# Performance work log

Measured on AMD Instinct MI355X. Metric: run time of the kernel, lower is better.

The kernel has to match this reference:

```python
import jax, jax.numpy as jnp
import numpy as np

N_NODES = 50000
IN_DIM = 128
HIDDEN = 64
OUT_DIM = 3
HEADS1 = 4
NEG_SLOPE = 0.2
EPS = 1e-16


def _glorot(key, shape):
    fan_in, fan_out = shape[0], shape[-1]
    lim = (6.0 / (fan_in + fan_out)) ** 0.5
    return jax.random.uniform(key, shape, jnp.float32, -lim, lim)


def setup_inputs() -> dict:
    key = jax.random.key(0)
    ks = jax.random.split(key, 12)
    x = jax.random.normal(ks[0], (N_NODES, IN_DIM), jnp.float32)
    edge_index = jax.random.randint(ks[1], (2, 400000), 0, N_NODES, jnp.int64)
    # layer 1: GATConv(in=128, out=64, heads=4)
    W1 = _glorot(ks[2], (IN_DIM, HEADS1 * HIDDEN))
    att_src1 = _glorot(ks[3], (HEADS1, HIDDEN))
    att_dst1 = _glorot(ks[4], (HEADS1, HIDDEN))
    b1 = jnp.zeros((HEADS1 * HIDDEN,), jnp.float32)
    # layer 2: GATConv(in=256, out=64, heads=1)
    W2 = _glorot(ks[5], (HEADS1 * HIDDEN, HIDDEN))
    att_src2 = _glorot(ks[6], (1, HIDDEN))
    att_dst2 = _glorot(ks[7], (1, HIDDEN))
    b2 = jnp.zeros((HIDDEN,), jnp.float32)
    # output linear
    Wout = _glorot(ks[8], (HIDDEN, OUT_DIM))
    bout = jnp.zeros((OUT_DIM,), jnp.float32)
    return {"x": x, "edge_index": edge_index, "W1": W1, "att_src1": att_src1,
            "att_dst1": att_dst1, "b1": b1, "W2": W2, "att_src2": att_src2,
            "att_dst2": att_dst2, "b2": b2, "Wout": Wout, "bout": bout}


def gat_conv(x, src, dst, W, a_src, a_dst, b, n_nodes):
    H, C = a_src.shape
    h = (x @ W).reshape(n_nodes, H, C)            # [N,H,C]
    a_s = jnp.sum(h * a_src[None], axis=-1)        # [N,H]
    a_d = jnp.sum(h * a_dst[None], axis=-1)        # [N,H]
    e = jax.nn.leaky_relu(a_s[src] + a_d[dst], NEG_SLOPE)  # [E,H]
    # segment softmax over incoming edges of each dst node
    m = jax.ops.segment_max(e, dst, num_segments=n_nodes)
    ex = jnp.exp(e - m[dst])
    denom = jax.ops.segment_sum(ex, dst, num_segments=n_nodes)
    alpha = ex / (denom[dst] + EPS)                # [E,H]
    msg = h[src] * alpha[..., None]                # [E,H,C]
    out = jax.ops.segment_sum(msg, dst, num_segments=n_nodes)
    return out.reshape(n_nodes, H * C) + b


def reference(x, edge_index, W1, att_src1, att_dst1, b1, W2, att_src2, att_dst2, b2, Wout, bout):
    n = x.shape[0]
    loop = jnp.arange(n, dtype=edge_index.dtype)
    src = jnp.concatenate([edge_index[0], loop])   # add self loops (PyG default)
    dst = jnp.concatenate([edge_index[1], loop])
    h = gat_conv(x, src, dst, W1, att_src1, att_dst1, b1, n)
    h = jax.nn.elu(h)
    h = gat_conv(h, src, dst, W2, att_src2, att_dst2, b2, n)
    h = jax.nn.elu(h)
    return h @ Wout + bout
```

## Files before the change

kernel.cpp:

```cpp
#include <hip/hip_runtime.h>
#include <hip/hip_bf16.h>
#include <math.h>

#define N_NODES  50000
#define IN_DIM   128
#define HIDDEN   64
#define OUT_DIM  3
#define HEADS1   4
#define E_RAW    400000
#define E_TOT    450000
#define NEG_SLOPE 0.2f
#define SCAN_CHUNK 1024
#define N_CHUNKS ((N_NODES + SCAN_CHUNK - 1) / SCAN_CHUNK)
#define WPREP_BLOCKS 128

typedef __attribute__((ext_vector_type(8))) short bf16x8;
typedef __attribute__((ext_vector_type(4))) float f32x4;

static __device__ __forceinline__ float bfu(unsigned short u) {
    return __uint_as_float(((unsigned)u) << 16);
}
static __device__ __forceinline__ unsigned short f2b_bits(float v) {
    __hip_bfloat16 b = __float2bfloat16(v);
    return *reinterpret_cast<unsigned short*>(&b);
}

static __device__ __forceinline__ void get_edge(const int* __restrict__ ei, int is64,
                                                int e, int& s, int& d) {
    if (e >= E_RAW) { s = d = e - E_RAW; return; }
    if (is64) { s = ei[2 * e]; d = ei[2 * E_RAW + 2 * e]; }
    else      { s = ei[e];     d = ei[E_RAW + e]; }
    s = min(max(s, 0), N_NODES - 1);
    d = min(max(d, 0), N_NODES - 1);
}

__global__ void detect_int64_kernel(const int* __restrict__ ei, int* __restrict__ flag) {
    __shared__ int any_nonzero;
    if (threadIdx.x == 0) any_nonzero = 0;
    __syncthreads();
    for (int i = threadIdx.x; i < 8192; i += blockDim.x) {
        int k = i * 48;
        if (ei[2 * k + 1] != 0) any_nonzero = 1;
    }
    __syncthreads();
    if (threadIdx.x == 0) flag[0] = (any_nonzero == 0) ? 1 : 0;
}

__global__ void wprep_count_kernel(const float* __restrict__ W1, __hip_bfloat16* __restrict__ W1T,
                                   const float* __restrict__ W2, __hip_bfloat16* __restrict__ W2T,
                                   const int* __restrict__ ei, const int* __restrict__ flag,
                                   int* __restrict__ deg) {
    int bid = blockIdx.x;
    if (bid < WPREP_BLOCKS) {
        int i = bid * 256 + threadIdx.x;
        if (i < 256 * 128) {
            int n = i >> 7, k = i & 127;
            *((unsigned short*)W1T + i) = f2b_bits(W1[k * 256 + n]);
        }
        if (i < 64 * 256) {
            int n = i >> 8, k = i & 255;
            *((unsigned short*)W2T + i) = f2b_bits(W2[k * 64 + n]);
        }
        return;
    }
    int e = (bid - WPREP_BLOCKS) * 256 + threadIdx.x;
    if (e >= E_TOT) return;
    int s, d;
    get_edge(ei, flag[0], e, s, d);
    atomicAdd(&deg[d], 1);
}

__global__ void scan_local_kernel(const int* __restrict__ deg, int* __restrict__ row_ptr,
                                  int* __restrict__ bsums) {
    __shared__ int buf[SCAN_CHUNK];
    int base = blockIdx.x * SCAN_CHUNK;
    int i = base + threadIdx.x;
    buf[threadIdx.x] = (i < N_NODES) ? deg[i] : 0;
    __syncthreads();
    for (int off = 1; off < SCAN_CHUNK; off <<= 1) {
        int t = (threadIdx.x >= off) ? buf[threadIdx.x - off] : 0;
        __syncthreads();
        buf[threadIdx.x] += t;
        __syncthreads();
    }
    if (i < N_NODES) row_ptr[i + 1] = buf[threadIdx.x];
    if (threadIdx.x == SCAN_CHUNK - 1) bsums[blockIdx.x] = buf[SCAN_CHUNK - 1];
    if (blockIdx.x == 0 && threadIdx.x == 0) row_ptr[0] = 0;
}

__global__ void scan_bsums_kernel(int* __restrict__ bsums) {
    __shared__ int buf[64];
    int i = threadIdx.x;
    buf[i] = (i < N_CHUNKS) ? bsums[i] : 0;
    __syncthreads();
    for (int off = 1; off < 64; off <<= 1) {
        int t = (i >= off) ? buf[i - off] : 0;
        __syncthreads();
        buf[i] += t;
        __syncthreads();
    }
    if (i < N_CHUNKS) bsums[i] = (i == 0) ? 0 : buf[i - 1];
}

__global__ void scan_add_kernel(int* __restrict__ row_ptr, const int* __restrict__ bsums,
                                const int* __restrict__ deg, int* __restrict__ cursor) {
    int i = blockIdx.x * blockDim.x + threadIdx.x;
    if (i < N_NODES) {
        int incl = row_ptr[i + 1] + bsums[i / SCAN_CHUNK];
        row_ptr[i + 1] = incl;
        cursor[i] = incl - deg[i];
    }
}

__global__ void scatter_kernel(const int* __restrict__ ei, const int* __restrict__ flag,
                               int* __restrict__ cursor, int* __restrict__ csr_src) {
    int e = blockIdx.x * blockDim.x + threadIdx.x;
    if (e >= E_TOT) return;
    int s, d;
    get_edge(ei, flag[0], e, s, d);
    int pos = atomicAdd(&cursor[d], 1);
    csr_src[pos] = s;
}

__global__ void __launch_bounds__(256) gemm_l1_mfma_kernel(
        const float* __restrict__ x, const __hip_bfloat16* __restrict__ W1T,
        const float* __restrict__ att_s, const float* __restrict__ att_d,
        __hip_bfloat16* __restrict__ h1,
        float* __restrict__ asb4, float* __restrict__ adb4) {
    __shared__ unsigned short As[16][136];
    const int tid = threadIdx.x;
    const int wave = tid >> 6, lane = tid & 63;
    const int quad = lane >> 4, m = lane & 15;
    const int row0 = blockIdx.x * 16;
    {
        int r = tid >> 4, seg = tid & 15;
        const float* xa = x + (size_t)(row0 + r) * IN_DIM + seg * 8;
        float4 u = *(const float4*)xa;
        float4 v = *(const float4*)(xa + 4);
        ushort4 p0, p1;
        p0.x = f2b_bits(u.x); p0.y = f2b_bits(u.y); p0.z = f2b_bits(u.z); p0.w = f2b_bits(u.w);
        p1.x = f2b_bits(v.x); p1.y = f2b_bits(v.y); p1.z = f2b_bits(v.z); p1.w = f2b_bits(v.w);
        *(ushort4*)&As[r][seg * 8]     = p0;
        *(ushort4*)&As[r][seg * 8 + 4] = p1;
    }
    __syncthreads();
    const int n0w = wave * 64;
    f32x4 acc0 = {0.f, 0.f, 0.f, 0.f}, acc1 = acc0, acc2 = acc0, acc3 = acc0;
    #pragma unroll
    for (int k0 = 0; k0 < IN_DIM; k0 += 32) {
        int kk = k0 + quad * 8;
        bf16x8 a = *(const bf16x8*)&As[m][kk];
        bf16x8 b0 = *(const bf16x8*)(W1T + (size_t)(n0w +  0 + m) * IN_DIM + kk);
        bf16x8 b1 = *(const bf16x8*)(W1T + (size_t)(n0w + 16 + m) * IN_DIM + kk);
        bf16x8 b2 = *(const bf16x8*)(W1T + (size_t)(n0w + 32 + m) * IN_DIM + kk);
        bf16x8 b3 = *(const bf16x8*)(W1T + (size_t)(n0w + 48 + m) * IN_DIM + kk);
        acc0 = __builtin_amdgcn_mfma_f32_16x16x32_bf16(a, b0, acc0, 0, 0, 0);
        acc1 = __builtin_amdgcn_mfma_f32_16x16x32_bf16(a, b1, acc1, 0, 0, 0);
        acc2 = __builtin_amdgcn_mfma_f32_16x16x32_bf16(a, b2, acc2, 0, 0, 0);
        acc3 = __builtin_amdgcn_mfma_f32_16x16x32_bf16(a, b3, acc3, 0, 0, 0);
    }
    float ats0 = att_s[n0w +  0 + m], atd0 = att_d[n0w +  0 + m];
    float ats1 = att_s[n0w + 16 + m], atd1 = att_d[n0w + 16 + m];
    float ats2 = att_s[n0w + 32 + m], atd2 = att_d[n0w + 32 + m];
    float ats3 = att_s[n0w + 48 + m], atd3 = att_d[n0w + 48 + m];
    unsigned short* out = (unsigned short*)h1;
    #pragma unroll
    for (int i = 0; i < 4; i++) {
        int grow = row0 + quad * 4 + i;
        size_t base = (size_t)grow * 256;
        out[base + n0w +  0 + m] = f2b_bits(acc0[i]);
        out[base + n0w + 16 + m] = f2b_bits(acc1[i]);
        out[base + n0w + 32 + m] = f2b_bits(acc2[i]);
        out[base + n0w + 48 + m] = f2b_bits(acc3[i]);
        float ps = acc0[i] * ats0 + acc1[i] * ats1 + acc2[i] * ats2 + acc3[i] * ats3;
        float pd = acc0[i] * atd0 + acc1[i] * atd1 + acc2[i] * atd2 + acc3[i] * atd3;
        #pragma unroll
        for (int off = 1; off < 16; off <<= 1) {
            ps += __shfl_xor(ps, off, 16);
            pd += __shfl_xor(pd, off, 16);
        }
        if (m == 0) {
            asb4[grow * 4 + wave] = ps;
            adb4[grow * 4 + wave] = pd;
        }
    }
}

__global__ void __launch_bounds__(256) gemm_l2_mfma_kernel(
        const __hip_bfloat16* __restrict__ eluagg, const __hip_bfloat16* __restrict__ W2T,
        const float* __restrict__ att_s, const float* __restrict__ att_d,
        __hip_bfloat16* __restrict__ h2,
        float* __restrict__ asb, float* __restrict__ adb) {
    __shared__ float sPS[4][16];
    __shared__ float sPD[4][16];
    const int tid = threadIdx.x;
    const int wave = tid >> 6, lane = tid & 63;
    const int quad = lane >> 4, m = lane & 15;
    const int row0 = blockIdx.x * 16;
    const int n0 = wave * 16;
    f32x4 acc = {0.f, 0.f, 0.f, 0.f};
    #pragma unroll
    for (int k0 = 0; k0 < 256; k0 += 32) {
        int kk = k0 + quad * 8;
        bf16x8 a = *(const bf16x8*)(eluagg + (size_t)(row0 + m) * 256 + kk);
        bf16x8 b = *(const bf16x8*)(W2T + (size_t)(n0 + m) * 256 + kk);
        acc = __builtin_amdgcn_mfma_f32_16x16x32_bf16(a, b, acc, 0, 0, 0);
    }
    float ats = att_s[n0 + m], atd = att_d[n0 + m];
    unsigned short* out = (unsigned short*)h2;
    #pragma unroll
    for (int i = 0; i < 4; i++) {
        int grow = row0 + quad * 4 + i;
        out[(size_t)grow * 64 + n0 + m] = f2b_bits(acc[i]);
        float ps = acc[i] * ats;
        float pd = acc[i] * atd;
        #pragma unroll
        for (int off = 1; off < 16; off <<= 1) {
            ps += __shfl_xor(ps, off, 16);
            pd += __shfl_xor(pd, off, 16);
        }
        if (m == 0) {
            sPS[wave][quad * 4 + i] = ps;
            sPD[wave][quad * 4 + i] = pd;
        }
    }
    __syncthreads();
    if (tid < 16) {
        float ps = sPS[0][tid] + sPS[1][tid] + sPS[2][tid] + sPS[3][tid];
        float pd = sPD[0][tid] + sPD[1][tid] + sPD[2][tid] + sPD[3][tid];
        asb[row0 + tid] = ps;
        adb[row0 + tid] = pd;
    }
}

__global__ void __launch_bounds__(256) gat_gather4_kernel(
        const int* __restrict__ row_ptr, const int* __restrict__ csr_src,
        const float* __restrict__ asb4, const float* __restrict__ adb4,
        const __hip_bfloat16* __restrict__ h1, const float* __restrict__ bias,
        __hip_bfloat16* __restrict__ eluagg) {
    int wave = threadIdx.x >> 6;
    int lane = threadIdx.x & 63;
    int n = blockIdx.x * 4 + wave;
    if (n >= N_NODES) return;
    int b = row_ptr[n], e = row_ptr[n + 1];
    const int c    = lane & 31;
    const int slot = lane >> 5;
    const int head = c >> 3;
    const int ei   = lane >> 2;
    const int hh   = lane & 3;
    float adnh = adb4[n * 4 + hh];
    float acc[8];
    #pragma unroll
    for (int i = 0; i < 8; i++) acc[i] = 0.f;
    float l = 0.f;
    for (int c0 = b; c0 < e; c0 += 16) {
        int cnt = min(16, e - c0);
        int s_all = (lane < cnt) ? csr_src[c0 + lane] : 0;
        int sE = __shfl(s_all, ei, 64);
        float w_all = 0.f;
        if (ei < cnt) {
            float v = asb4[sE * 4 + hh] + adnh;
            v = (v > 0.f) ? v : NEG_SLOPE * v;
            w_all = __expf(v);
        }
        #pragma unroll 2
        for (int k = 0; k < cnt; k += 2) {
            int eidx = k + slot;
            int s = __shfl(s_all, eidx, 64);
            float w = __shfl(w_all, eidx * 4 + head, 64);
            bf16x8 f = *(const bf16x8*)(h1 + (size_t)s * 256 + c * 8);
            l += w;
            #pragma unroll
            for (int i = 0; i < 8; i++)
                acc[i] += w * bfu((unsigned short)f[i]);
        }
    }
    #pragma unroll
    for (int i = 0; i < 8; i++) acc[i] += __shfl_xor(acc[i], 32, 64);
    l += __shfl_xor(l, 32, 64);
    if (lane < 32) {
        float il = 1.f / (l + 1e-16f);
        float4 b0 = *(const float4*)(bias + c * 8);
        float4 b1 = *(const float4*)(bias + c * 8 + 4);
        float r[8];
        r[0] = acc[0] * il + b0.x; r[1] = acc[1] * il + b0.y;
        r[2] = acc[2] * il + b0.z; r[3] = acc[3] * il + b0.w;
        r[4] = acc[4] * il + b1.x; r[5] = acc[5] * il + b1.y;
        r[6] = acc[6] * il + b1.z; r[7] = acc[7] * il + b1.w;
        bf16x8 st;
        #pragma unroll
        for (int i = 0; i < 8; i++) {
            float v = (r[i] > 0.f) ? r[i] : expm1f(r[i]);
            st[i] = (short)f2b_bits(v);
        }
        *(bf16x8*)(eluagg + (size_t)n * 256 + c * 8) = st;
    }
}

__global__ void __launch_bounds__(256) gat_gather1_out_kernel(
        const int* __restrict__ row_ptr, const int* __restrict__ csr_src,
        const float* __restrict__ asb, const float* __restrict__ adb,
        const __hip_bfloat16* __restrict__ h2, const float* __restrict__ bias,
        const float* __restrict__ Wout, const float* __restrict__ bout,
        float* __restrict__ out) {
    int wave = threadIdx.x >> 6;
    int lane = threadIdx.x & 63;
    int n = blockIdx.x * 4 + wave;
    if (n >= N_NODES) return;
    int b = row_ptr[n], e = row_ptr[n + 1];
    const int c    = lane & 7;
    const int slot = lane >> 3;
    float adn = adb[n];
    float acc[8];
    #pragma unroll
    for (int i = 0; i < 8; i++) acc[i] = 0.f;
    float l = 0.f;
    for (int c0 = b; c0 < e; c0 += 64) {
        int cnt = min(64, e - c0);
        int s_all = (lane < cnt) ? csr_src[c0 + lane] : 0;
        float w_all = 0.f;
        if (lane < cnt) {
            float v = asb[s_all] + adn;
            v = (v > 0.f) ? v : NEG_SLOPE * v;
            w_all = __expf(v);
        }
        #pragma unroll 2
        for (int k = 0; k < cnt; k += 8) {
            int eidx = k + slot;
            int s = __shfl(s_all, eidx, 64);
            float w = __shfl(w_all, eidx, 64);
            bf16x8 f = *(const bf16x8*)(h2 + (size_t)s * 64 + c * 8);
            l += w;
            #pragma unroll
            for (int i = 0; i < 8; i++)
                acc[i] += w * bfu((unsigned short)f[i]);
        }
    }
    #pragma unroll
    for (int off = 8; off < 64; off <<= 1) {
        #pragma unroll
        for (int i = 0; i < 8; i++) acc[i] += __shfl_xor(acc[i], off, 64);
        l += __shfl_xor(l, off, 64);
    }
    float il = 1.f / (l + 1e-16f);
    float4 b0 = *(const float4*)(bias + c * 8);
    float4 b1 = *(const float4*)(bias + c * 8 + 4);
    float v[8];
    v[0] = acc[0] * il + b0.x; v[1] = acc[1] * il + b0.y;
    v[2] = acc[2] * il + b0.z; v[3] = acc[3] * il + b0.w;
    v[4] = acc[4] * il + b1.x; v[5] = acc[5] * il + b1.y;
    v[6] = acc[6] * il + b1.z; v[7] = acc[7] * il + b1.w;
    #pragma unroll
    for (int i = 0; i < 8; i++) v[i] = (v[i] > 0.f) ? v[i] : expm1f(v[i]);
    const float* wp = Wout + c * 24;
    float o0 = 0.f, o1 = 0.f, o2 = 0.f;
    #pragma unroll
    for (int i = 0; i < 8; i++) {
        o0 += v[i] * wp[i * 3 + 0];
        o1 += v[i] * wp[i * 3 + 1];
        o2 += v[i] * wp[i * 3 + 2];
    }
    #pragma unroll
    for (int off = 1; off < 8; off <<= 1) {
        o0 += __shfl_xor(o0, off, 64);
        o1 += __shfl_xor(o1, off, 64);
        o2 += __shfl_xor(o2, off, 64);
    }
    if (lane == 0) {
        out[n * OUT_DIM + 0] = o0 + bout[0];
        out[n * OUT_DIM + 1] = o1 + bout[1];
        out[n * OUT_DIM + 2] = o2 + bout[2];
    }
}

extern "C" void kernel_launch(void* const* d_in, const int* in_sizes, int n_in,
                              void* d_out, int out_size, void* d_ws, size_t ws_size,
                              hipStream_t stream) {
    const float* x    = (const float*)d_in[0];
    const int*   ei   = (const int*)d_in[1];
    const float* W1   = (const float*)d_in[2];
    const float* as1  = (const float*)d_in[3];
    const float* ad1  = (const float*)d_in[4];
    const float* b1   = (const float*)d_in[5];
    const float* W2   = (const float*)d_in[6];
    const float* as2  = (const float*)d_in[7];
    const float* ad2  = (const float*)d_in[8];
    const float* b2v  = (const float*)d_in[9];
    const float* Wout = (const float*)d_in[10];
    const float* bout = (const float*)d_in[11];
    float* out = (float*)d_out;

    float* ws    = (float*)d_ws;
    int*   flag  = (int*)ws;
    float* asb4  = ws + 16;
    float* adb4  = asb4 + (size_t)N_NODES * 4;
    float* asb1  = adb4 + (size_t)N_NODES * 4;
    float* adb1  = asb1 + N_NODES;
    __hip_bfloat16* h1     = (__hip_bfloat16*)(adb1 + N_NODES);
    __hip_bfloat16* eluagg = (__hip_bfloat16*)(h1 + (size_t)N_NODES * 256);
    __hip_bfloat16* h2     = (__hip_bfloat16*)(eluagg + (size_t)N_NODES * 256);
    __hip_bfloat16* W1T    = (__hip_bfloat16*)(h2 + (size_t)N_NODES * 64);
    __hip_bfloat16* W2T    = W1T + 256 * 128;
    int* deg     = (int*)(W2T + 64 * 256);
    int* bsums   = deg + N_NODES;
    int* row_ptr = bsums + 64;
    int* cursor  = row_ptr + N_NODES + 16;
    int* csr_src = cursor + N_NODES;

    const int EB = (E_TOT + 255) / 256;
    const int NB = (N_NODES + 255) / 256;
    const int AB = (N_NODES + 3) / 4;
    const int MB = N_NODES / 16;

    detect_int64_kernel<<<1, 256, 0, stream>>>(ei, flag);
    hipMemsetAsync(deg, 0, (size_t)N_NODES * sizeof(int), stream);

    wprep_count_kernel<<<WPREP_BLOCKS + EB, 256, 0, stream>>>(W1, W1T, W2, W2T, ei, flag, deg);
    scan_local_kernel<<<N_CHUNKS, SCAN_CHUNK, 0, stream>>>(deg, row_ptr, bsums);
    scan_bsums_kernel<<<1, 64, 0, stream>>>(bsums);
    scan_add_kernel<<<NB, 256, 0, stream>>>(row_ptr, bsums, deg, cursor);
    scatter_kernel<<<EB, 256, 0, stream>>>(ei, flag, cursor, csr_src);

    gemm_l1_mfma_kernel<<<MB, 256, 0, stream>>>(x, W1T, as1, ad1, h1, asb4, adb4);
    gat_gather4_kernel<<<AB, 256, 0, stream>>>(row_ptr, csr_src, asb4, adb4, h1, b1, eluagg);

    gemm_l2_mfma_kernel<<<MB, 256, 0, stream>>>(eluagg, W2T, as2, ad2, h2, asb1, adb1);
    gat_gather1_out_kernel<<<AB, 256, 0, stream>>>(row_ptr, csr_src, asb1, adb1, h2,
                                                   b2v, Wout, bout, out);
}
```

Measured before the change: 284.9 us.

## Store layer-1 features head-major and split gather blocks per head

The layer-1 GEMM now writes h1 and the attention logits in a head-major layout ([head][node][64] and [head][node]). The gather kernel gets one block per (head, 8-node group), so each wave reads 128-byte rows from a single head's plane. The intent is to shrink the working set that must stay in cache per pass, at the cost of 4x more blocks and an extra cross-lane reduction. The int64-detection kernel is also parallelised across 32 blocks, with a memset initialising the flag.

Measured after the change: 326.5 us. 1.15x slower.

```diff
diff --git a/kernel.cpp b/kernel.cpp
--- a/kernel.cpp
+++ b/kernel.cpp
@@ -13,6 +13,7 @@
 #define SCAN_CHUNK 1024
 #define N_CHUNKS ((N_NODES + SCAN_CHUNK - 1) / SCAN_CHUNK)
 #define WPREP_BLOCKS 128
+#define G4_BLOCKS 50000
 
 typedef __attribute__((ext_vector_type(8))) short bf16x8;
 typedef __attribute__((ext_vector_type(4))) float f32x4;
@@ -35,15 +36,9 @@
 }
 
 __global__ void detect_int64_kernel(const int* __restrict__ ei, int* __restrict__ flag) {
-    __shared__ int any_nonzero;
-    if (threadIdx.x == 0) any_nonzero = 0;
-    __syncthreads();
-    for (int i = threadIdx.x; i < 8192; i += blockDim.x) {
-        int k = i * 48;
-        if (ei[2 * k + 1] != 0) any_nonzero = 1;
-    }
-    __syncthreads();
-    if (threadIdx.x == 0) flag[0] = (any_nonzero == 0) ? 1 : 0;
+    int i = blockIdx.x * blockDim.x + threadIdx.x;
+    int k = i * 48;
+    if (ei[2 * k + 1] != 0) flag[0] = 0;
 }
 
 __global__ void wprep_count_kernel(const float* __restrict__ W1, __hip_bfloat16* __restrict__ W1T,
@@ -164,14 +159,15 @@
     float ats2 = att_s[n0w + 32 + m], atd2 = att_d[n0w + 32 + m];
     float ats3 = att_s[n0w + 48 + m], atd3 = att_d[n0w + 48 + m];
     unsigned short* out = (unsigned short*)h1;
+    const size_t hbase = (size_t)wave * N_NODES * 64;
     #pragma unroll
     for (int i = 0; i < 4; i++) {
         int grow = row0 + quad * 4 + i;
-        size_t base = (size_t)grow * 256;
-        out[base + n0w +  0 + m] = f2b_bits(acc0[i]);
-        out[base + n0w + 16 + m] = f2b_bits(acc1[i]);
-        out[base + n0w + 32 + m] = f2b_bits(acc2[i]);
-        out[base + n0w + 48 + m] = f2b_bits(acc3[i]);
+        size_t base = hbase + (size_t)grow * 64;
+        out[base +  0 + m] = f2b_bits(acc0[i]);
+        out[base + 16 + m] = f2b_bits(acc1[i]);
+        out[base + 32 + m] = f2b_bits(acc2[i]);
+        out[base + 48 + m] = f2b_bits(acc3[i]);
         float ps = acc0[i] * ats0 + acc1[i] * ats1 + acc2[i] * ats2 + acc3[i] * ats3;
         float pd = acc0[i] * atd0 + acc1[i] * atd1 + acc2[i] * atd2 + acc3[i] * atd3;
         #pragma unroll
@@ -180,8 +176,8 @@
             pd += __shfl_xor(pd, off, 16);
         }
         if (m == 0) {
-            asb4[grow * 4 + wave] = ps;
-            adb4[grow * 4 + wave] = pd;
+            asb4[(size_t)wave * N_NODES + grow] = ps;
+            adb4[(size_t)wave * N_NODES + grow] = pd;
         }
     }
 }
@@ -236,39 +232,42 @@
 __global__ void __launch_bounds__(256) gat_gather4_kernel(
         const int* __restrict__ row_ptr, const int* __restrict__ csr_src,
         const float* __restrict__ asb4, const float* __restrict__ adb4,
-        const __hip_bfloat16* __restrict__ h1, const float* __restrict__ bias,
+        const __hip_bfloat16* __restrict__ h1,
+        const float* __restrict__ bias,
         __hip_bfloat16* __restrict__ eluagg) {
-    int wave = threadIdx.x >> 6;
-    int lane = threadIdx.x & 63;
-    int n = blockIdx.x * 4 + wave;
+    const int bid  = blockIdx.x;
+    const int x    = bid & 7;
+    const int head = x >> 1;
+    const int nb   = (bid >> 3) * 2 + (x & 1);
+    const int wave = threadIdx.x >> 6;
+    const int lane = threadIdx.x & 63;
+    const int n = nb * 4 + wave;
     if (n >= N_NODES) return;
     int b = row_ptr[n], e = row_ptr[n + 1];
-    const int c    = lane & 31;
-    const int slot = lane >> 5;
-    const int head = c >> 3;
-    const int ei   = lane >> 2;
-    const int hh   = lane & 3;
-    float adnh = adb4[n * 4 + hh];
+    const int c    = lane & 7;
+    const int slot = lane >> 3;
+    const __hip_bfloat16* h1h = h1 + (size_t)head * N_NODES * 64;
+    const float* asbh = asb4 + (size_t)head * N_NODES;
+    const float adn = adb4[(size_t)head * N_NODES + n];
     float acc[8];
     #pragma unroll
     for (int i = 0; i < 8; i++) acc[i] = 0.f;
     float l = 0.f;
-    for (int c0 = b; c0 < e; c0 += 16) {
-        int cnt = min(16, e - c0);
+    for (int c0 = b; c0 < e; c0 += 64) {
+        int cnt = min(64, e - c0);
         int s_all = (lane < cnt) ? csr_src[c0 + lane] : 0;
-        int sE = __shfl(s_all, ei, 64);
         float w_all = 0.f;
-        if (ei < cnt) {
-            float v = asb4[sE * 4 + hh] + adnh;
+        if (lane < cnt) {
+            float v = asbh[s_all] + adn;
             v = (v > 0.f) ? v : NEG_SLOPE * v;
             w_all = __expf(v);
         }
         #pragma unroll 2
-        for (int k = 0; k < cnt; k += 2) {
+        for (int k = 0; k < cnt; k += 8) {
             int eidx = k + slot;
             int s = __shfl(s_all, eidx, 64);
-            float w = __shfl(w_all, eidx * 4 + head, 64);
-            bf16x8 f = *(const bf16x8*)(h1 + (size_t)s * 256 + c * 8);
+            float w = __shfl(w_all, eidx, 64);
+            bf16x8 f = *(const bf16x8*)(h1h + (size_t)s * 64 + c * 8);
             l += w;
             #pragma unroll
             for (int i = 0; i < 8; i++)
@@ -276,12 +275,15 @@
         }
     }
     #pragma unroll
-    for (int i = 0; i < 8; i++) acc[i] += __shfl_xor(acc[i], 32, 64);
-    l += __shfl_xor(l, 32, 64);
-    if (lane < 32) {
+    for (int off = 8; off < 64; off <<= 1) {
+        #pragma unroll
+        for (int i = 0; i < 8; i++) acc[i] += __shfl_xor(acc[i], off, 64);
+        l += __shfl_xor(l, off, 64);
+    }
+    if (lane < 8) {
         float il = 1.f / (l + 1e-16f);
-        float4 b0 = *(const float4*)(bias + c * 8);
-        float4 b1 = *(const float4*)(bias + c * 8 + 4);
+        float4 b0 = *(const float4*)(bias + head * 64 + c * 8);
+        float4 b1 = *(const float4*)(bias + head * 64 + c * 8 + 4);
         float r[8];
         r[0] = acc[0] * il + b0.x; r[1] = acc[1] * il + b0.y;
         r[2] = acc[2] * il + b0.z; r[3] = acc[3] * il + b0.w;
@@ -293,7 +295,7 @@
             float v = (r[i] > 0.f) ? r[i] : expm1f(r[i]);
             st[i] = (short)f2b_bits(v);
         }
-        *(bf16x8*)(eluagg + (size_t)n * 256 + c * 8) = st;
+        *(bf16x8*)(eluagg + (size_t)n * 256 + head * 64 + c * 8) = st;
     }
 }
 
@@ -412,7 +414,8 @@
     const int AB = (N_NODES + 3) / 4;
     const int MB = N_NODES / 16;
 
-    detect_int64_kernel<<<1, 256, 0, stream>>>(ei, flag);
+    hipMemsetAsync(flag, 1, 4, stream);
+    detect_int64_kernel<<<32, 256, 0, stream>>>(ei, flag);
     hipMemsetAsync(deg, 0, (size_t)N_NODES * sizeof(int), stream);
 
     wprep_count_kernel<<<WPREP_BLOCKS + EB, 256, 0, stream>>>(W1, W1T, W2, W2T, ei, flag, deg);
@@ -422,7 +425,7 @@
     scatter_kernel<<<EB, 256, 0, stream>>>(ei, flag, cursor, csr_src);
 
     gemm_l1_mfma_kernel<<<MB, 256, 0, stream>>>(x, W1T, as1, ad1, h1, asb4, adb4);
-    gat_gather4_kernel<<<AB, 256, 0, stream>>>(row_ptr, csr_src, asb4, adb4, h1, b1, eluagg);
+    gat_gather4_kernel<<<G4_BLOCKS, 256, 0, stream>>>(row_ptr, csr_src, asb4, adb4, h1, b1, eluagg);
 
     gemm_l2_mfma_kernel<<<MB, 256, 0, stream>>>(eluagg, W2T, as2, ad2, h2, asb1, adb1);
     gat_gather1_out_kernel<<<AB, 256, 0, stream>>>(row_ptr, csr_src, asb1, adb1, h2,
```

## Fuse layer-1 gather with layer-2 GEMM and fold small scan/memset kernels

Applied to the files above, without the earlier changes.

Layer-1 attention aggregation now runs inside the layer-2 GEMM kernel. Each block aggregates 16 nodes into shared memory and feeds them straight to MFMA, so the 25.6MB eluagg intermediate is never written to or read back from global memory. The degree memset is folded into the int64-detect kernel, and the bsums scan is moved into scan_add via wave shuffles, removing two launches. The cost is that each block now handles 16 nodes sequentially, four per wave, which lowers parallelism during the latency-bound gather phase and adds a block barrier before the MFMA.

Measured after the change: 267.7 us. -6.1%, faster.

```diff
diff --git a/kernel.cpp b/kernel.cpp
--- a/kernel.cpp
+++ b/kernel.cpp
@@ -34,16 +34,24 @@
     d = min(max(d, 0), N_NODES - 1);
 }
 
-__global__ void detect_int64_kernel(const int* __restrict__ ei, int* __restrict__ flag) {
-    __shared__ int any_nonzero;
-    if (threadIdx.x == 0) any_nonzero = 0;
-    __syncthreads();
-    for (int i = threadIdx.x; i < 8192; i += blockDim.x) {
-        int k = i * 48;
-        if (ei[2 * k + 1] != 0) any_nonzero = 1;
-    }
-    __syncthreads();
-    if (threadIdx.x == 0) flag[0] = (any_nonzero == 0) ? 1 : 0;
+__global__ void detect_zero_kernel(const int* __restrict__ ei, int* __restrict__ flag,
+                                   int* __restrict__ deg) {
+    int gid = blockIdx.x * 256 + threadIdx.x;
+    for (int i = gid; i < N_NODES; i += 64 * 256) deg[i] = 0;
+    if (blockIdx.x == 0) {
+        int nz = 0;
+        #pragma unroll 4
+        for (int t = 0; t < 32; t++) {
+            int k = (threadIdx.x * 32 + t) * 48;
+            nz |= ei[2 * k + 1];
+        }
+        __shared__ int s;
+        if (threadIdx.x == 0) s = 0;
+        __syncthreads();
+        if (__any(nz != 0) && (threadIdx.x & 63) == 0) s = 1;
+        __syncthreads();
+        if (threadIdx.x == 0) flag[0] = s ? 0 : 1;
+    }
 }
 
 __global__ void wprep_count_kernel(const float* __restrict__ W1, __hip_bfloat16* __restrict__ W1T,
@@ -88,25 +96,24 @@
     if (blockIdx.x == 0 && threadIdx.x == 0) row_ptr[0] = 0;
 }
 
-__global__ void scan_bsums_kernel(int* __restrict__ bsums) {
-    __shared__ int buf[64];
-    int i = threadIdx.x;
-    buf[i] = (i < N_CHUNKS) ? bsums[i] : 0;
-    __syncthreads();
-    for (int off = 1; off < 64; off <<= 1) {
-        int t = (i >= off) ? buf[i - off] : 0;
-        __syncthreads();
-        buf[i] += t;
-        __syncthreads();
-    }
-    if (i < N_CHUNKS) bsums[i] = (i == 0) ? 0 : buf[i - 1];
-}
-
 __global__ void scan_add_kernel(int* __restrict__ row_ptr, const int* __restrict__ bsums,
                                 const int* __restrict__ deg, int* __restrict__ cursor) {
+    __shared__ int soff[64];
+    if (threadIdx.x < 64) {
+        int v = (threadIdx.x < N_CHUNKS) ? bsums[threadIdx.x] : 0;
+        #pragma unroll
+        for (int off = 1; off < 64; off <<= 1) {
+            int t = __shfl_up(v, off, 64);
+            if (threadIdx.x >= off) v += t;
+        }
+        soff[threadIdx.x] = v;
+    }
+    __syncthreads();
     int i = blockIdx.x * blockDim.x + threadIdx.x;
     if (i < N_NODES) {
-        int incl = row_ptr[i + 1] + bsums[i / SCAN_CHUNK];
+        int ch = i / SCAN_CHUNK;
+        int add = (ch == 0) ? 0 : soff[ch - 1];
+        int incl = row_ptr[i + 1] + add;
         row_ptr[i + 1] = incl;
         cursor[i] = incl - deg[i];
     }
@@ -186,25 +193,88 @@
     }
 }
 
-__global__ void __launch_bounds__(256) gemm_l2_mfma_kernel(
-        const __hip_bfloat16* __restrict__ eluagg, const __hip_bfloat16* __restrict__ W2T,
+__global__ void __launch_bounds__(256) gat_gather4_l2_kernel(
+        const int* __restrict__ row_ptr, const int* __restrict__ csr_src,
+        const float* __restrict__ asb4, const float* __restrict__ adb4,
+        const __hip_bfloat16* __restrict__ h1, const float* __restrict__ bias,
+        const __hip_bfloat16* __restrict__ W2T,
         const float* __restrict__ att_s, const float* __restrict__ att_d,
         __hip_bfloat16* __restrict__ h2,
         float* __restrict__ asb, float* __restrict__ adb) {
+    __shared__ unsigned short As[16][264];
     __shared__ float sPS[4][16];
     __shared__ float sPD[4][16];
     const int tid = threadIdx.x;
     const int wave = tid >> 6, lane = tid & 63;
+    const int row0 = blockIdx.x * 16;
+    const int c    = lane & 31;
+    const int slot = lane >> 5;
+    const int head = c >> 3;
+    const int eidx0 = lane >> 2;
+    const int hh   = lane & 3;
+
+    for (int g = 0; g < 4; g++) {
+        const int n = row0 + wave * 4 + g;
+        int b = row_ptr[n], e = row_ptr[n + 1];
+        float adnh = adb4[n * 4 + hh];
+        float acc[8];
+        #pragma unroll
+        for (int i = 0; i < 8; i++) acc[i] = 0.f;
+        float l = 0.f;
+        for (int c0 = b; c0 < e; c0 += 16) {
+            int cnt = min(16, e - c0);
+            int s_all = (lane < cnt) ? csr_src[c0 + lane] : 0;
+            int sE = __shfl(s_all, eidx0, 64);
+            float w_all = 0.f;
+            if (eidx0 < cnt) {
+                float v = asb4[sE * 4 + hh] + adnh;
+                v = (v > 0.f) ? v : NEG_SLOPE * v;
+                w_all = __expf(v);
+            }
+            #pragma unroll 2
+            for (int k = 0; k < cnt; k += 2) {
+                int eidx = k + slot;
+                int s = __shfl(s_all, eidx, 64);
+                float w = __shfl(w_all, eidx * 4 + head, 64);
+                bf16x8 f = *(const bf16x8*)(h1 + (size_t)s * 256 + c * 8);
+                l += w;
+                #pragma unroll
+                for (int i = 0; i < 8; i++)
+                    acc[i] += w * bfu((unsigned short)f[i]);
+            }
+        }
+        #pragma unroll
+        for (int i = 0; i < 8; i++) acc[i] += __shfl_xor(acc[i], 32, 64);
+        l += __shfl_xor(l, 32, 64);
+        if (lane < 32) {
+            float il = 1.f / (l + 1e-16f);
+            float4 b0 = *(const float4*)(bias + c * 8);
+            float4 b1 = *(const float4*)(bias + c * 8 + 4);
+            float r[8];
+            r[0] = acc[0] * il + b0.x; r[1] = acc[1] * il + b0.y;
+            r[2] = acc[2] * il + b0.z; r[3] = acc[3] * il + b0.w;
+            r[4] = acc[4] * il + b1.x; r[5] = acc[5] * il + b1.y;
+            r[6] = acc[6] * il + b1.z; r[7] = acc[7] * il + b1.w;
+            bf16x8 st;
+            #pragma unroll
+            for (int i = 0; i < 8; i++) {
+                float v = (r[i] > 0.f) ? r[i] : expm1f(r[i]);
+                st[i] = (short)f2b_bits(v);
+            }
+            *(bf16x8*)&As[wave * 4 + g][c * 8] = st;
+        }
+    }
+    __syncthreads();
+
     const int quad = lane >> 4, m = lane & 15;
-    const int row0 = blockIdx.x * 16;
     const int n0 = wave * 16;
     f32x4 acc = {0.f, 0.f, 0.f, 0.f};
     #pragma unroll
     for (int k0 = 0; k0 < 256; k0 += 32) {
         int kk = k0 + quad * 8;
-        bf16x8 a = *(const bf16x8*)(eluagg + (size_t)(row0 + m) * 256 + kk);
-        bf16x8 b = *(const bf16x8*)(W2T + (size_t)(n0 + m) * 256 + kk);
-        acc = __builtin_amdgcn_mfma_f32_16x16x32_bf16(a, b, acc, 0, 0, 0);
+        bf16x8 a = *(const bf16x8*)&As[m][kk];
+        bf16x8 bfr = *(const bf16x8*)(W2T + (size_t)(n0 + m) * 256 + kk);
+        acc = __builtin_amdgcn_mfma_f32_16x16x32_bf16(a, bfr, acc, 0, 0, 0);
     }
     float ats = att_s[n0 + m], atd = att_d[n0 + m];
     unsigned short* out = (unsigned short*)h2;
@@ -230,70 +300,6 @@
         float pd = sPD[0][tid] + sPD[1][tid] + sPD[2][tid] + sPD[3][tid];
         asb[row0 + tid] = ps;
         adb[row0 + tid] = pd;
-    }
-}
-
-__global__ void __launch_bounds__(256) gat_gather4_kernel(
-        const int* __restrict__ row_ptr, const int* __restrict__ csr_src,
-        const float* __restrict__ asb4, const float* __restrict__ adb4,
-        const __hip_bfloat16* __restrict__ h1, const float* __restrict__ bias,
-        __hip_bfloat16* __restrict__ eluagg) {
-    int wave = threadIdx.x >> 6;
-    int lane = threadIdx.x & 63;
-    int n = blockIdx.x * 4 + wave;
-    if (n >= N_NODES) return;
-    int b = row_ptr[n], e = row_ptr[n + 1];
-    const int c    = lane & 31;
-    const int slot = lane >> 5;
-    const int head = c >> 3;
-    const int ei   = lane >> 2;
-    const int hh   = lane & 3;
-    float adnh = adb4[n * 4 + hh];
-    float acc[8];
-    #pragma unroll
-    for (int i = 0; i < 8; i++) acc[i] = 0.f;
-    float l = 0.f;
-    for (int c0 = b; c0 < e; c0 += 16) {
-        int cnt = min(16, e - c0);
-        int s_all = (lane < cnt) ? csr_src[c0 + lane] : 0;
-        int sE = __shfl(s_all, ei, 64);
-        float w_all = 0.f;
-        if (ei < cnt) {
-            float v = asb4[sE * 4 + hh] + adnh;
-            v = (v > 0.f) ? v : NEG_SLOPE * v;
-            w_all = __expf(v);
-        }
-        #pragma unroll 2
-        for (int k = 0; k < cnt; k += 2) {
-            int eidx = k + slot;
-            int s = __shfl(s_all, eidx, 64);
-            float w = __shfl(w_all, eidx * 4 + head, 64);
-            bf16x8 f = *(const bf16x8*)(h1 + (size_t)s * 256 + c * 8);
-            l += w;
-            #pragma unroll
-            for (int i = 0; i < 8; i++)
-                acc[i] += w * bfu((unsigned short)f[i]);
-        }
-    }
-    #pragma unroll
-    for (int i = 0; i < 8; i++) acc[i] += __shfl_xor(acc[i], 32, 64);
-    l += __shfl_xor(l, 32, 64);
-    if (lane < 32) {
-        float il = 1.f / (l + 1e-16f);
-        float4 b0 = *(const float4*)(bias + c * 8);
-        float4 b1 = *(const float4*)(bias + c * 8 + 4);
-        float r[8];
-        r[0] = acc[0] * il + b0.x; r[1] = acc[1] * il + b0.y;
-        r[2] = acc[2] * il + b0.z; r[3] = acc[3] * il + b0.w;
-        r[4] = acc[4] * il + b1.x; r[5] = acc[5] * il + b1.y;
-        r[6] = acc[6] * il + b1.z; r[7] = acc[7] * il + b1.w;
-        bf16x8 st;
-        #pragma unroll
-        for (int i = 0; i < 8; i++) {
-            float v = (r[i] > 0.f) ? r[i] : expm1f(r[i]);
-            st[i] = (short)f2b_bits(v);
-        }
-        *(bf16x8*)(eluagg + (size_t)n * 256 + c * 8) = st;
     }
 }
 
@@ -397,8 +403,7 @@
     float* asb1  = adb4 + (size_t)N_NODES * 4;
     float* adb1  = asb1 + N_NODES;
     __hip_bfloat16* h1     = (__hip_bfloat16*)(adb1 + N_NODES);
-    __hip_bfloat16* eluagg = (__hip_bfloat16*)(h1 + (size_t)N_NODES * 256);
-    __hip_bfloat16* h2     = (__hip_bfloat16*)(eluagg + (size_t)N_NODES * 256);
+    __hip_bfloat16* h2     = (__hip_bfloat16*)(h1 + (size_t)N_NODES * 256);
     __hip_bfloat16* W1T    = (__hip_bfloat16*)(h2 + (size_t)N_NODES * 64);
     __hip_bfloat16* W2T    = W1T + 256 * 128;
     int* deg     = (int*)(W2T + 64 * 256);
@@ -412,19 +417,17 @@
     const int AB = (N_NODES + 3) / 4;
     const int MB = N_NODES / 16;
 
-    detect_int64_kernel<<<1, 256, 0, stream>>>(ei, flag);
-    hipMemsetAsync(deg, 0, (size_t)N_NODES * sizeof(int), stream);
-
+    detect_zero_kernel<<<64, 256, 0, stream>>>(ei, flag, deg);
     wprep_count_kernel<<<WPREP_BLOCKS + EB, 256, 0, stream>>>(W1, W1T, W2, W2T, ei, flag, deg);
     scan_local_kernel<<<N_CHUNKS, SCAN_CHUNK, 0, stream>>>(deg, row_ptr, bsums);
-    scan_bsums_kernel<<<1, 64, 0, stream>>>(bsums);
     scan_add_kernel<<<NB, 256, 0, stream>>>(row_ptr, bsums, deg, cursor);
     scatter_kernel<<<EB, 256, 0, stream>>>(ei, flag, cursor, csr_src);
 
     gemm_l1_mfma_kernel<<<MB, 256, 0, stream>>>(x, W1T, as1, ad1, h1, asb4, adb4);
-    gat_gather4_kernel<<<AB, 256, 0, stream>>>(row_ptr, csr_src, asb4, adb4, h1, b1, eluagg);
-
-    gemm_l2_mfma_kernel<<<MB, 256, 0, stream>>>(eluagg, W2T, as2, ad2, h2, asb1, adb1);
+
+    gat_gather4_l2_kernel<<<MB, 256, 0, stream>>>(row_ptr, csr_src, asb4, adb4, h1, b1,
+                                                  W2T, as2, ad2, h2, asb1, adb1);
+
     gat_gather1_out_kernel<<<AB, 256, 0, stream>>>(row_ptr, csr_src, asb1, adb1, h2,
                                                    b2v, Wout, bout, out);
 }
```

## Merge preprocessing kernels: per-block int64 detect, single-block scan, fused scatter+GEMM1

Applied to the files above, without the earlier changes.

Drops the separate int64-detection kernel; each edge block now infers the index width from the high words of its own edges. The three-kernel multi-block prefix scan becomes one single-block kernel that walks the degree array in 49 chunks using wave shuffles and a running carry. The CSR scatter is merged into the layer-1 GEMM launch as extra blocks so the two overlap. This removes several launches and serialization points, but the single-block scan runs serially over 50k entries. Per-block width detection may also be wrong if a block's high words happen to be all zero.

Measured after the change: 297.3 us. +4.3%, slower.

```diff
diff --git a/kernel.cpp b/kernel.cpp
--- a/kernel.cpp
+++ b/kernel.cpp
@@ -10,9 +10,9 @@
 #define E_RAW    400000
 #define E_TOT    450000
 #define NEG_SLOPE 0.2f
-#define SCAN_CHUNK 1024
-#define N_CHUNKS ((N_NODES + SCAN_CHUNK - 1) / SCAN_CHUNK)
 #define WPREP_BLOCKS 128
+#define EB_SC ((E_TOT + 255) / 256)
+#define MB_GE (N_NODES / 16)
 
 typedef __attribute__((ext_vector_type(8))) short bf16x8;
 typedef __attribute__((ext_vector_type(4))) float f32x4;
@@ -34,22 +34,21 @@
     d = min(max(d, 0), N_NODES - 1);
 }
 
-__global__ void detect_int64_kernel(const int* __restrict__ ei, int* __restrict__ flag) {
-    __shared__ int any_nonzero;
-    if (threadIdx.x == 0) any_nonzero = 0;
+static __device__ __forceinline__ int block_is64(const int* __restrict__ ei,
+                                                 int e, bool valid, int* nzbuf) {
+    bool real = valid && (e < E_RAW);
+    int hv = real ? ei[2 * e + 1] : 0;
+    if (threadIdx.x == 0) *nzbuf = 0;
     __syncthreads();
-    for (int i = threadIdx.x; i < 8192; i += blockDim.x) {
-        int k = i * 48;
-        if (ei[2 * k + 1] != 0) any_nonzero = 1;
-    }
+    if (__any(hv != 0) && (threadIdx.x & 63) == 0) *nzbuf = 1;
     __syncthreads();
-    if (threadIdx.x == 0) flag[0] = (any_nonzero == 0) ? 1 : 0;
+    return (*nzbuf == 0);
 }
 
 __global__ void wprep_count_kernel(const float* __restrict__ W1, __hip_bfloat16* __restrict__ W1T,
                                    const float* __restrict__ W2, __hip_bfloat16* __restrict__ W2T,
-                                   const int* __restrict__ ei, const int* __restrict__ flag,
-                                   int* __restrict__ deg) {
+                                   const int* __restrict__ ei, int* __restrict__ deg) {
+    __shared__ int nz;
     int bid = blockIdx.x;
     if (bid < WPREP_BLOCKS) {
         int i = bid * 256 + threadIdx.x;
@@ -64,74 +63,72 @@
         return;
     }
     int e = (bid - WPREP_BLOCKS) * 256 + threadIdx.x;
-    if (e >= E_TOT) return;
+    bool valid = e < E_TOT;
+    int is64 = block_is64(ei, e, valid, &nz);
+    if (!valid) return;
     int s, d;
-    get_edge(ei, flag[0], e, s, d);
+    get_edge(ei, is64, e, s, d);
     atomicAdd(&deg[d], 1);
 }
 
-__global__ void scan_local_kernel(const int* __restrict__ deg, int* __restrict__ row_ptr,
-                                  int* __restrict__ bsums) {
-    __shared__ int buf[SCAN_CHUNK];
-    int base = blockIdx.x * SCAN_CHUNK;
-    int i = base + threadIdx.x;
-    buf[threadIdx.x] = (i < N_NODES) ? deg[i] : 0;
-    __syncthreads();
-    for (int off = 1; off < SCAN_CHUNK; off <<= 1) {
-        int t = (threadIdx.x >= off) ? buf[threadIdx.x - off] : 0;
+__global__ void scan_all_kernel(const int* __restrict__ deg, int* __restrict__ row_ptr,
+                                int* __restrict__ cursor) {
+    __shared__ int wsum[4];
+    const int t = threadIdx.x, wv = t >> 6, ln = t & 63;
+    int carry = 0;
+    if (t == 0) row_ptr[0] = 0;
+    for (int chunk = 0; chunk < 49; ++chunk) {
+        int g = chunk * 256 + t;
+        int4 d = (g < 12500) ? ((const int4*)deg)[g] : make_int4(0, 0, 0, 0);
+        int p0 = d.x, p1 = p0 + d.y, p2 = p1 + d.z, p3 = p2 + d.w;
+        int s = p3;
+        #pragma unroll
+        for (int off = 1; off < 64; off <<= 1) {
+            int u = __shfl_up(s, off, 64);
+            if (ln >= off) s += u;
+        }
+        if (ln == 63) wsum[wv] = s;
         __syncthreads();
-        buf[threadIdx.x] += t;
+        int wbase = carry;
+        #pragma unroll
+        for (int w = 0; w < 4; w++) wbase += (w < wv) ? wsum[w] : 0;
+        int ex = wbase + s - p3;
+        if (g < 12500) {
+            int i = g * 4;
+            row_ptr[i + 1] = ex + p0; row_ptr[i + 2] = ex + p1;
+            row_ptr[i + 3] = ex + p2; row_ptr[i + 4] = ex + p3;
+            cursor[i]     = ex;       cursor[i + 1]  = ex + p0;
+            cursor[i + 2] = ex + p1;  cursor[i + 3]  = ex + p2;
+        }
+        carry += wsum[0] + wsum[1] + wsum[2] + wsum[3];
         __syncthreads();
     }
-    if (i < N_NODES) row_ptr[i + 1] = buf[threadIdx.x];
-    if (threadIdx.x == SCAN_CHUNK - 1) bsums[blockIdx.x] = buf[SCAN_CHUNK - 1];
-    if (blockIdx.x == 0 && threadIdx.x == 0) row_ptr[0] = 0;
-}
-
-__global__ void scan_bsums_kernel(int* __restrict__ bsums) {
-    __shared__ int buf[64];
-    int i = threadIdx.x;
-    buf[i] = (i < N_CHUNKS) ? bsums[i] : 0;
-    __syncthreads();
-    for (int off = 1; off < 64; off <<= 1) {
-        int t = (i >= off) ? buf[i - off] : 0;
-        __syncthreads();
-        buf[i] += t;
-        __syncthreads();
-    }
-    if (i < N_CHUNKS) bsums[i] = (i == 0) ? 0 : buf[i - 1];
-}
-
-__global__ void scan_add_kernel(int* __restrict__ row_ptr, const int* __restrict__ bsums,
-                                const int* __restrict__ deg, int* __restrict__ cursor) {
-    int i = blockIdx.x * blockDim.x + threadIdx.x;
-    if (i < N_NODES) {
-        int incl = row_ptr[i + 1] + bsums[i / SCAN_CHUNK];
-        row_ptr[i + 1] = incl;
-        cursor[i] = incl - deg[i];
-    }
-}
-
-__global__ void scatter_kernel(const int* __restrict__ ei, const int* __restrict__ flag,
-                               int* __restrict__ cursor, int* __restrict__ csr_src) {
-    int e = blockIdx.x * blockDim.x + threadIdx.x;
-    if (e >= E_TOT) return;
-    int s, d;
-    get_edge(ei, flag[0], e, s, d);
-    int pos = atomicAdd(&cursor[d], 1);
-    csr_src[pos] = s;
-}
-
-__global__ void __launch_bounds__(256) gemm_l1_mfma_kernel(
+}
+
+__global__ void __launch_bounds__(256) scatter_gemm_l1_kernel(
+        const int* __restrict__ ei,
+        int* __restrict__ cursor, int* __restrict__ csr_src,
         const float* __restrict__ x, const __hip_bfloat16* __restrict__ W1T,
         const float* __restrict__ att_s, const float* __restrict__ att_d,
         __hip_bfloat16* __restrict__ h1,
         float* __restrict__ asb4, float* __restrict__ adb4) {
     __shared__ unsigned short As[16][136];
+    __shared__ int nz;
+    if (blockIdx.x < EB_SC) {
+        int e = blockIdx.x * 256 + threadIdx.x;
+        bool valid = e < E_TOT;
+        int is64 = block_is64(ei, e, valid, &nz);
+        if (!valid) return;
+        int s, d;
+        get_edge(ei, is64, e, s, d);
+        int pos = atomicAdd(&cursor[d], 1);
+        csr_src[pos] = s;
+        return;
+    }
     const int tid = threadIdx.x;
     const int wave = tid >> 6, lane = tid & 63;
     const int quad = lane >> 4, m = lane & 15;
-    const int row0 = blockIdx.x * 16;
+    const int row0 = (blockIdx.x - EB_SC) * 16;
     {
         int r = tid >> 4, seg = tid & 15;
         const float* xa = x + (size_t)(row0 + r) * IN_DIM + seg * 8;
@@ -183,53 +180,6 @@
             asb4[grow * 4 + wave] = ps;
             adb4[grow * 4 + wave] = pd;
         }
-    }
-}
-
-__global__ void __launch_bounds__(256) gemm_l2_mfma_kernel(
-        const __hip_bfloat16* __restrict__ eluagg, const __hip_bfloat16* __restrict__ W2T,
-        const float* __restrict__ att_s, const float* __restrict__ att_d,
-        __hip_bfloat16* __restrict__ h2,
-        float* __restrict__ asb, float* __restrict__ adb) {
-    __shared__ float sPS[4][16];
-    __shared__ float sPD[4][16];
-    const int tid = threadIdx.x;
-    const int wave = tid >> 6, lane = tid & 63;
-    const int quad = lane >> 4, m = lane & 15;
-    const int row0 = blockIdx.x * 16;
-    const int n0 = wave * 16;
-    f32x4 acc = {0.f, 0.f, 0.f, 0.f};
-    #pragma unroll
-    for (int k0 = 0; k0 < 256; k0 += 32) {
-        int kk = k0 + quad * 8;
-        bf16x8 a = *(const bf16x8*)(eluagg + (size_t)(row0 + m) * 256 + kk);
-        bf16x8 b = *(const bf16x8*)(W2T + (size_t)(n0 + m) * 256 + kk);
-        acc = __builtin_amdgcn_mfma_f32_16x16x32_bf16(a, b, acc, 0, 0, 0);
-    }
-    float ats = att_s[n0 + m], atd = att_d[n0 + m];
-    unsigned short* out = (unsigned short*)h2;
-    #pragma unroll
-    for (int i = 0; i < 4; i++) {
-        int grow = row0 + quad * 4 + i;
-        out[(size_t)grow * 64 + n0 + m] = f2b_bits(acc[i]);
-        float ps = acc[i] * ats;
-        float pd = acc[i] * atd;
-        #pragma unroll
-        for (int off = 1; off < 16; off <<= 1) {
-            ps += __shfl_xor(ps, off, 16);
-            pd += __shfl_xor(pd, off, 16);
-        }
-        if (m == 0) {
-            sPS[wave][quad * 4 + i] = ps;
-            sPD[wave][quad * 4 + i] = pd;
-        }
-    }
-    __syncthreads();
-    if (tid < 16) {
-        float ps = sPS[0][tid] + sPS[1][tid] + sPS[2][tid] + sPS[3][tid];
-        float pd = sPD[0][tid] + sPD[1][tid] + sPD[2][tid] + sPD[3][tid];
-        asb[row0 + tid] = ps;
-        adb[row0 + tid] = pd;
     }
 }
 
@@ -297,6 +247,53 @@
     }
 }
 
+__global__ void __launch_bounds__(256) gemm_l2_mfma_kernel(
+        const __hip_bfloat16* __restrict__ eluagg, const __hip_bfloat16* __restrict__ W2T,
+        const float* __restrict__ att_s, const float* __restrict__ att_d,
+        __hip_bfloat16* __restrict__ h2,
+        float* __restrict__ asb, float* __restrict__ adb) {
+    __shared__ float sPS[4][16];
+    __shared__ float sPD[4][16];
+    const int tid = threadIdx.x;
+    const int wave = tid >> 6, lane = tid & 63;
+    const int quad = lane >> 4, m = lane & 15;
+    const int row0 = blockIdx.x * 16;
+    const int n0 = wave * 16;
+    f32x4 acc = {0.f, 0.f, 0.f, 0.f};
+    #pragma unroll
+    for (int k0 = 0; k0 < 256; k0 += 32) {
+        int kk = k0 + quad * 8;
+        bf16x8 a = *(const bf16x8*)(eluagg + (size_t)(row0 + m) * 256 + kk);
+        bf16x8 b = *(const bf16x8*)(W2T + (size_t)(n0 + m) * 256 + kk);
+        acc = __builtin_amdgcn_mfma_f32_16x16x32_bf16(a, b, acc, 0, 0, 0);
+    }
+    float ats = att_s[n0 + m], atd = att_d[n0 + m];
+    unsigned short* out = (unsigned short*)h2;
+    #pragma unroll
+    for (int i = 0; i < 4; i++) {
+        int grow = row0 + quad * 4 + i;
+        out[(size_t)grow * 64 + n0 + m] = f2b_bits(acc[i]);
+        float ps = acc[i] * ats;
+        float pd = acc[i] * atd;
+        #pragma unroll
+        for (int off = 1; off < 16; off <<= 1) {
+            ps += __shfl_xor(ps, off, 16);
+            pd += __shfl_xor(pd, off, 16);
+        }
+        if (m == 0) {
+            sPS[wave][quad * 4 + i] = ps;
+            sPD[wave][quad * 4 + i] = pd;
+        }
+    }
+    __syncthreads();
+    if (tid < 16) {
+        float ps = sPS[0][tid] + sPS[1][tid] + sPS[2][tid] + sPS[3][tid];
+        float pd = sPD[0][tid] + sPD[1][tid] + sPD[2][tid] + sPD[3][tid];
+        asb[row0 + tid] = ps;
+        adb[row0 + tid] = pd;
+    }
+}
+
 __global__ void __launch_bounds__(256) gat_gather1_out_kernel(
         const int* __restrict__ row_ptr, const int* __restrict__ csr_src,
         const float* __restrict__ asb, const float* __restrict__ adb,
@@ -391,7 +388,6 @@
     float* out = (float*)d_out;
 
     float* ws    = (float*)d_ws;
-    int*   flag  = (int*)ws;
     float* asb4  = ws + 16;
     float* adb4  = asb4 + (size_t)N_NODES * 4;
     float* asb1  = adb4 + (size_t)N_NODES * 4;
@@ -402,29 +398,24 @@
     __hip_bfloat16* W1T    = (__hip_bfloat16*)(h2 + (size_t)N_NODES * 64);
     __hip_bfloat16* W2T    = W1T + 256 * 128;
     int* deg     = (int*)(W2T + 64 * 256);
-    int* bsums   = deg + N_NODES;
-    int* row_ptr = bsums + 64;
+    int* row_ptr = deg + N_NODES;
     int* cursor  = row_ptr + N_NODES + 16;
     int* csr_src = cursor + N_NODES;
 
-    const int EB = (E_TOT + 255) / 256;
-    const int NB = (N_NODES + 255) / 256;
+    const int EB = EB_SC;
     const int AB = (N_NODES + 3) / 4;
-    const int MB = N_NODES / 16;
-
-    detect_int64_kernel<<<1, 256, 0, stream>>>(ei, flag);
+
     hipMemsetAsync(deg, 0, (size_t)N_NODES * sizeof(int), stream);
-
-    wprep_count_kernel<<<WPREP_BLOCKS + EB, 256, 0, stream>>>(W1, W1T, W2, W2T, ei, flag, deg);
-    scan_local_kernel<<<N_CHUNKS, SCAN_CHUNK, 0, stream>>>(deg, row_ptr, bsums);
-    scan_bsums_kernel<<<1, 64, 0, stream>>>(bsums);
-    scan_add_kernel<<<NB, 256, 0, stream>>>(row_ptr, bsums, deg, cursor);
-    scatter_kernel<<<EB, 256, 0, stream>>>(ei, flag, cursor, csr_src);
-
-    gemm_l1_mfma_kernel<<<MB, 256, 0, stream>>>(x, W1T, as1, ad1, h1, asb4, adb4);
+    wprep_count_kernel<<<WPREP_BLOCKS + EB, 256, 0, stream>>>(W1, W1T, W2, W2T, ei, deg);
+    scan_all_kernel<<<1, 256, 0, stream>>>(deg, row_ptr, cursor);
+
+    scatter_gemm_l1_kernel<<<EB + MB_GE, 256, 0, stream>>>(ei, cursor, csr_src,
+                                                           x, W1T, as1, ad1, h1, asb4, adb4);
+
     gat_gather4_kernel<<<AB, 256, 0, stream>>>(row_ptr, csr_src, asb4, adb4, h1, b1, eluagg);
 
-    gemm_l2_mfma_kernel<<<MB, 256, 0, stream>>>(eluagg, W2T, as2, ad2, h2, asb1, adb1);
+    gemm_l2_mfma_kernel<<<MB_GE, 256, 0, stream>>>(eluagg, W2T, as2, ad2, h2, asb1, adb1);
+
     gat_gather1_out_kernel<<<AB, 256, 0, stream>>>(row_ptr, csr_src, asb1, adb1, h2,
                                                    b2v, Wout, bout, out);
 }
```
